# Optimization experiments

Measured on AMD Instinct MI355X. Metric: run time of the kernel, lower is better.

Reference implementation:

```python
import jax, jax.numpy as jnp
import numpy as np

N_HEADS = 8
N_LAYERS = 2
LN_EPS = 1e-5


def _mha(x, Win, bin_, Wout, bout):
    # torch nn.MultiheadAttention, eval mode (dropout off). x: [b, s, d]
    b, s, d = x.shape
    dh = d // N_HEADS
    qkv = x @ Win.T + bin_                      # [b, s, 3d]
    q, k, v = jnp.split(qkv, 3, axis=-1)
    q = q.reshape(b, s, N_HEADS, dh)
    k = k.reshape(b, s, N_HEADS, dh)
    v = v.reshape(b, s, N_HEADS, dh)
    scores = jnp.einsum('bqhd,bkhd->bhqk', q, k) / jnp.sqrt(jnp.asarray(dh, x.dtype))
    attn = jax.nn.softmax(scores, axis=-1)
    o = jnp.einsum('bhqk,bkhd->bqhd', attn, v).reshape(b, s, d)
    return o @ Wout.T + bout


def _layer_norm(x, g, b):
    mu = jnp.mean(x, axis=-1, keepdims=True)
    var = jnp.mean(jnp.square(x - mu), axis=-1, keepdims=True)
    return (x - mu) * jax.lax.rsqrt(var + LN_EPS) * g + b


def _vertex_conv(feat, inc, prev, Win, bin_, Wout, bout, Wproj, ln_g, ln_b, alpha):
    # feat: [b,m,d], inc: [b,m,e]
    attn = _mha(feat, Win, bin_, Wout, bout)              # [b,m,d]
    scores = jnp.einsum('bme,bmd->bed', inc, attn)        # incidence aggregation
    w = jax.nn.softmax(scores, axis=1)                    # softmax over edges
    # fused form of einsum('bme,bmd->bmed') then einsum('bmed,bed->bed')
    edge = scores * w                                     # [b,e,d]
    edge = edge @ Wproj.T                                 # no-bias projection
    edge = _layer_norm(edge, ln_g, ln_b)
    if prev is not None:
        edge = alpha * prev + (1.0 - alpha) * edge
        edge = edge + prev
    return edge


def _edge_conv(inc, edge_feat, prev, Win, bin_, Wout, bout, Wproj, ln_g, ln_b, alpha):
    # inc: [b,m,e], edge_feat: [b,e,d]
    _ = _mha(edge_feat, Win, bin_, Wout, bout)            # attn computed, output unused downstream
    wef = jnp.einsum('bed,bme->bmd', edge_feat, inc)      # edge->node aggregation
    node = wef @ Wproj.T
    node = _layer_norm(node, ln_g, ln_b)
    if prev is not None:
        node = alpha * prev + (1.0 - alpha) * node
        node = node + prev
    return node


def setup_inputs() -> dict:
    key = jax.random.key(0)
    ks = jax.random.split(key, 8)
    b, m, e, d = 8, 1024, 1536, 256
    s = 0.02
    return {
        'features': jax.random.normal(ks[0], (b, m, d), jnp.float32),
        'inc_mat': (jax.random.uniform(ks[1], (b, m, e), jnp.float32) < 0.05).astype(jnp.float32),
        'vc_Win': jax.random.normal(ks[2], (3 * d, d), jnp.float32) * s,
        'vc_bin': jnp.zeros((3 * d,), jnp.float32),
        'vc_Wout': jax.random.normal(ks[3], (d, d), jnp.float32) * s,
        'vc_bout': jnp.zeros((d,), jnp.float32),
        'vc_Wproj': jax.random.normal(ks[4], (d, d), jnp.float32) * s,
        'vc_ln_g': jnp.ones((d,), jnp.float32),
        'vc_ln_b': jnp.zeros((d,), jnp.float32),
        'vc_alpha': jnp.asarray(0.5, jnp.float32),
        'ec_Win': jax.random.normal(ks[5], (3 * d, d), jnp.float32) * s,
        'ec_bin': jnp.zeros((3 * d,), jnp.float32),
        'ec_Wout': jax.random.normal(ks[6], (d, d), jnp.float32) * s,
        'ec_bout': jnp.zeros((d,), jnp.float32),
        'ec_Wproj': jax.random.normal(ks[7], (d, d), jnp.float32) * s,
        'ec_ln_g': jnp.ones((d,), jnp.float32),
        'ec_ln_b': jnp.zeros((d,), jnp.float32),
        'ec_alpha': jnp.asarray(0.5, jnp.float32),
    }


def reference(features, inc_mat,
              vc_Win, vc_bin, vc_Wout, vc_bout, vc_Wproj, vc_ln_g, vc_ln_b, vc_alpha,
              ec_Win, ec_bin, ec_Wout, ec_bout, ec_Wproj, ec_ln_g, ec_ln_b, ec_alpha):
    vc = (vc_Win, vc_bin, vc_Wout, vc_bout, vc_Wproj, vc_ln_g, vc_ln_b, vc_alpha)
    ec = (ec_Win, ec_bin, ec_Wout, ec_bout, ec_Wproj, ec_ln_g, ec_ln_b, ec_alpha)
    edge_feats = _vertex_conv(features, inc_mat, None, *vc)
    node_feats = _edge_conv(inc_mat, edge_feats, features, *ec)
    for _ in range(N_LAYERS):  # shared weights across layers, as in the torch module
        edge_feats = _vertex_conv(features, inc_mat, edge_feats, *vc)
        node_feats = _edge_conv(inc_mat, edge_feats, node_feats, *ec)
    return node_feats, edge_feats, inc_mat
```

## Files before the change

kernel.cpp:

```cpp
#include <hip/hip_runtime.h>
#include <stdint.h>


#define DEV static __device__ __forceinline__

typedef __attribute__((ext_vector_type(8))) short bf16x8;
typedef __attribute__((ext_vector_type(4))) float f32x4;

DEV uint16_t f2bf(float x){
  union{float f; uint32_t u;} v; v.f=x;
  uint32_t r = v.u + 0x7fffu + ((v.u>>16)&1u);
  return (uint16_t)(r>>16);
}
DEV float bf2f(uint16_t b){
  union{uint32_t u; float f;} v; v.u=((uint32_t)b)<<16; return v.f;
}

DEV uint32_t cvtpk_bf16(float lo, float hi){
  uint32_t d;
  asm("v_cvt_pk_bf16_f32 %0, %1, %2" : "=v"(d) : "v"(lo), "v"(hi));
  return d;
}

#if __has_builtin(__builtin_amdgcn_exp2f)
DEV float exp2fast(float x){ return __builtin_amdgcn_exp2f(x); }
#else
DEV float exp2fast(float x){ return __expf(x * 0.6931471805599453f); }
#endif

#if __has_builtin(__builtin_amdgcn_global_load_lds)
#define HAVE_GLL 1
#else
#define HAVE_GLL 0
#endif

DEV void load_lds16(const uint16_t* g, void* l){
#if HAVE_GLL
  __builtin_amdgcn_global_load_lds((const __attribute__((address_space(1))) uint32_t*)g,
                                   (__attribute__((address_space(3))) uint32_t*)l, 16, 0, 0);
#else
  *(bf16x8*)l = *(const bf16x8*)g;
#endif
}

__global__ __launch_bounds__(256)
void prep(const float* __restrict__ inc, float* __restrict__ out_inc,
          uint16_t* __restrict__ incb, uint16_t* __restrict__ incT,
          const float* __restrict__ feats, const float* __restrict__ win,
          const float* __restrict__ wout, const float* __restrict__ wpv,
          const float* __restrict__ wpe,
          uint16_t* __restrict__ xb, uint16_t* __restrict__ ow,
          uint16_t* __restrict__ oo, uint16_t* __restrict__ ov,
          uint16_t* __restrict__ oe){
  __shared__ float T[32][33];
  int bx = blockIdx.x;
  int tid = threadIdx.x;
  if (bx < 12288){
    int x = bx % 48;
    int t = bx / 48;
    int y = t % 32;
    int b = t / 32;
    int c0 = x*32, r0 = y*32;
    int tx = tid & 31, ty = tid >> 5;
    size_t base = (size_t)b*1024*1536;
#pragma unroll
    for (int j=0;j<4;++j){
      int r = r0 + ty + j*8;
      size_t idx = base + (size_t)r*1536 + c0 + tx;
      float v = inc[idx];
      T[ty+j*8][tx] = v;
      out_inc[idx] = v;
      incb[idx] = f2bf(v);
    }
    __syncthreads();
    size_t baseT = (size_t)b*1536*1024;
#pragma unroll
    for (int j=0;j<4;++j){
      int c = c0 + ty + j*8;
      incT[baseT + (size_t)c*1024 + r0 + tx] = f2bf(T[tx][ty+j*8]);
    }
  } else {
    int i = (bx - 12288)*256 + tid;
    const float* src; uint16_t* dst; int j;
    if (i < 524288){ src=feats; dst=xb; j=i; }
    else {
      i -= 524288;
      if (i < 49152){ src=win; dst=ow; j=i; }
      else if (i < 65536){ src=wout; dst=oo; j=i-49152; }
      else if (i < 81920){ src=wpv; dst=ov; j=i-65536; }
      else { src=wpe; dst=oe; j=i-81920; }
    }
    float4 v = ((const float4*)src)[j];
    union { uint16_t u[4]; uint64_t q; } p;
    p.u[0]=f2bf(v.x); p.u[1]=f2bf(v.y); p.u[2]=f2bf(v.z); p.u[3]=f2bf(v.w);
    ((uint64_t*)dst)[j] = p.q;
  }
}

template<int WM, int BK, int EPI>
__global__ __launch_bounds__(256, 3)
void gemm_nt(const uint16_t* __restrict__ A, const uint16_t* __restrict__ B,
             float* __restrict__ Cf, uint16_t* __restrict__ Cb,
             const float* __restrict__ bias,
             int M, int N, int K, long sA, long sB, long sC,
             float* __restrict__ extra){
  constexpr int AROWS = WM*32;
  constexpr int UPR = BK/8;
  constexpr int RPP = 256/UPR;
  __shared__ short As[AROWS*BK];
  __shared__ short Bs[128*BK];
  const int tid = threadIdx.x;
  const int lane = tid & 63;
  const int w = tid >> 6;
  const int wm = w & 1, wn = w >> 1;
  const int r = lane & 15, q = lane >> 4;
  const long zb = blockIdx.z;
  const uint16_t* Ab = A + zb*sA + (size_t)(blockIdx.x*AROWS)*K;
  const uint16_t* Bb = B + zb*sB + (size_t)(blockIdx.y*128)*K;
  f32x4 acc[WM][4];
#pragma unroll
  for (int i=0;i<WM;++i)
#pragma unroll
    for (int j=0;j<4;++j) acc[i][j] = (f32x4){0.f,0.f,0.f,0.f};

  const int srow = tid / UPR;
  const int sblk = tid % UPR;

  for (int kb = 0; kb < K; kb += BK){
#pragma unroll
    for (int i=0;i<AROWS/RPP;++i){
      int row = srow + RPP*i;
      int lblk = sblk ^ (row & (UPR-1));
      load_lds16(Ab + (size_t)row*K + kb + lblk*8, (char*)As + i*4096 + tid*16);
    }
#pragma unroll
    for (int i=0;i<128/RPP;++i){
      int row = srow + RPP*i;
      int lblk = sblk ^ (row & (UPR-1));
      load_lds16(Bb + (size_t)row*K + kb + lblk*8, (char*)Bs + i*4096 + tid*16);
    }
    __syncthreads();
#pragma unroll
    for (int kc=0;kc<BK/32;++kc){
      bf16x8 af[WM], bf[4];
#pragma unroll
      for (int mt=0;mt<WM;++mt){
        int m = wm*(WM*16) + mt*16 + r;
        af[mt] = *(const bf16x8*)&As[m*BK + ((kc*4 + q) ^ (m&(UPR-1)))*8];
      }
#pragma unroll
      for (int nt=0;nt<4;++nt){
        int n = wn*64 + nt*16 + r;
        bf[nt] = *(const bf16x8*)&Bs[n*BK + ((kc*4 + q) ^ (n&(UPR-1)))*8];
      }
#pragma unroll
      for (int mt=0;mt<WM;++mt)
#pragma unroll
        for (int nt=0;nt<4;++nt)
          acc[mt][nt] = __builtin_amdgcn_mfma_f32_16x16x32_bf16(af[mt], bf[nt], acc[mt][nt], 0,0,0);
    }
    __syncthreads();
  }

  const int gm0 = blockIdx.x*AROWS + wm*(WM*16);
  const int gn0 = blockIdx.y*128 + wn*64;

  if constexpr (EPI == 1){
#pragma unroll
    for (int mt=0;mt<WM;++mt){
      int gmb = gm0 + mt*16 + q*4;
      size_t bb_ = (size_t)(gmb>>10)*(256*1024);
      int mm = gmb & 1023;
#pragma unroll
      for (int nt=0;nt<4;++nt){
        int gn = gn0 + nt*16 + r;
        float bv = bias ? bias[gn] : 0.f;
        union{uint16_t u[4]; uint64_t q64;} pk;
#pragma unroll
        for (int reg=0;reg<4;++reg) pk.u[reg] = f2bf(acc[mt][nt][reg] + bv);
        *(uint64_t*)(Cb + bb_ + (size_t)gn*1024 + mm) = pk.q64;
      }
    }
  } else {
#pragma unroll
    for (int mt=0;mt<WM;++mt){
#pragma unroll
      for (int nt=0;nt<4;++nt){
        int gn = gn0 + nt*16 + r;
        float bv = bias ? bias[gn] : 0.f;
#pragma unroll
        for (int reg=0;reg<4;++reg){
          int gm = gm0 + mt*16 + q*4 + reg;
          float v = acc[mt][nt][reg] + bv;
          size_t off = (size_t)(zb*sC) + (size_t)gm*N + gn;
          if (Cf) Cf[off] = v;
          if (Cb) Cb[off] = f2bf(v);
        }
      }
    }
  }
  (void)extra;
}

__global__ __launch_bounds__(256, 4)
void gemm_score(const uint16_t* __restrict__ A,
                const uint16_t* __restrict__ B,
                float* __restrict__ part,
                uint16_t* __restrict__ VE){
  __shared__ short As[32*64];
  __shared__ short Bs[256*64];
  const int tid = threadIdx.x;
  const int lane = tid & 63;
  const int w = tid >> 6;
  const int r = lane & 15, q = lane >> 4;
  const int bx = (blockIdx.x & 7)*48 + (blockIdx.x >> 3);
  const int batch = bx / 48;
  const uint16_t* Ab = A + (size_t)bx*32*1024;
  const uint16_t* Bb = B + (size_t)batch*256*1024;

  f32x4 acc[2][4];
#pragma unroll
  for (int i=0;i<2;++i)
#pragma unroll
    for (int j=0;j<4;++j) acc[i][j] = (f32x4){0.f,0.f,0.f,0.f};

  const int srow = tid >> 3;
  const int sblk = tid & 7;

  for (int kb = 0; kb < 1024; kb += 64){
    { int lblk = sblk ^ (srow & 7);
      load_lds16(Ab + (size_t)srow*1024 + kb + lblk*8, (char*)As + tid*16); }
#pragma unroll
    for (int i=0;i<8;++i){
      int row = srow + 32*i;
      int lblk = sblk ^ (row & 7);
      load_lds16(Bb + (size_t)row*1024 + kb + lblk*8, (char*)Bs + i*4096 + tid*16);
    }
    __syncthreads();
#pragma unroll
    for (int kc=0;kc<2;++kc){
      bf16x8 af[2], bf[4];
#pragma unroll
      for (int mt=0;mt<2;++mt){
        int m = mt*16 + r;
        af[mt] = *(const bf16x8*)&As[m*64 + ((kc*4 + q) ^ (m&7))*8];
      }
#pragma unroll
      for (int nt=0;nt<4;++nt){
        int n = w*64 + nt*16 + r;
        bf[nt] = *(const bf16x8*)&Bs[n*64 + ((kc*4 + q) ^ (n&7))*8];
      }
#pragma unroll
      for (int mt=0;mt<2;++mt)
#pragma unroll
        for (int nt=0;nt<4;++nt)
          acc[mt][nt] = __builtin_amdgcn_mfma_f32_16x16x32_bf16(af[mt], bf[nt], acc[mt][nt], 0,0,0);
    }
    __syncthreads();
  }

#pragma unroll
  for (int nt=0;nt<4;++nt){
    int gn = w*64 + nt*16 + r;
    float s = 0.f;
#pragma unroll
    for (int mt=0;mt<2;++mt){
#pragma unroll
      for (int reg=0;reg<4;++reg){
        float v = acc[mt][nt][reg];
        float ev = __expf(v);
        s += ev;
        int row = mt*16 + q*4 + reg;
        VE[(size_t)(bx*32 + row)*256 + gn] = f2bf(v*ev);
      }
    }
    s += __shfl_xor(s, 16);
    s += __shfl_xor(s, 32);
    if (q == 0) part[(size_t)bx*256 + gn] = s;
  }
}

__global__ __launch_bounds__(256, 4)
void gemm_ln_edge(const uint16_t* __restrict__ SB, const uint16_t* __restrict__ B,
                  const float* __restrict__ part, const float* __restrict__ g,
                  const float* __restrict__ bb, const float* __restrict__ alpha,
                  float* __restrict__ out, uint16_t* __restrict__ baset){
  __shared__ short As[32*64];
  __shared__ short Bs[256*64];
  __shared__ float lnS[4][32], lnQ[4][32];
  __shared__ float PLinv[256];
  const int tid = threadIdx.x;
  const int lane = tid & 63;
  const int w = tid >> 6;
  const int r = lane & 15, q = lane >> 4;
  const int bx = (blockIdx.x & 7)*48 + (blockIdx.x >> 3);
  const int batch = bx / 48;

  {
    float s = 0.f;
#pragma unroll
    for (int i=0;i<48;++i) s += part[((size_t)batch*48 + i)*256 + tid];
    PLinv[tid] = 1.0f / s;
  }
  __syncthreads();

  f32x4 acc[2][4];
#pragma unroll
  for (int i=0;i<2;++i)
#pragma unroll
    for (int j=0;j<4;++j) acc[i][j] = (f32x4){0.f,0.f,0.f,0.f};

  const int srow = tid >> 3;
  const int sblk = tid & 7;

  for (int kb = 0; kb < 256; kb += 64){
    {
      bf16x8 v = *(const bf16x8*)(SB + (size_t)(bx*32 + srow)*256 + kb + sblk*8);
      const float* Lp = &PLinv[kb + sblk*8];
      float xv[8];
#pragma unroll
      for (int j=0;j<8;++j) xv[j] = bf2f((uint16_t)v[j]) * Lp[j];
      union{uint32_t u[4]; bf16x8 v8;} pk;
      pk.u[0] = cvtpk_bf16(xv[0], xv[1]);
      pk.u[1] = cvtpk_bf16(xv[2], xv[3]);
      pk.u[2] = cvtpk_bf16(xv[4], xv[5]);
      pk.u[3] = cvtpk_bf16(xv[6], xv[7]);
      *(bf16x8*)&As[srow*64 + (sblk ^ (srow&7))*8] = pk.v8;
    }
#pragma unroll
    for (int i=0;i<8;++i){
      int row = srow + 32*i;
      int lblk = sblk ^ (row & 7);
      load_lds16(B + (size_t)row*256 + kb + lblk*8, (char*)Bs + i*4096 + tid*16);
    }
    __syncthreads();
#pragma unroll
    for (int kc=0;kc<2;++kc){
      bf16x8 af[2], bf[4];
#pragma unroll
      for (int mt=0;mt<2;++mt){
        int m = mt*16 + r;
        af[mt] = *(const bf16x8*)&As[m*64 + ((kc*4 + q) ^ (m&7))*8];
      }
#pragma unroll
      for (int nt=0;nt<4;++nt){
        int n = w*64 + nt*16 + r;
        bf[nt] = *(const bf16x8*)&Bs[n*64 + ((kc*4 + q) ^ (n&7))*8];
      }
#pragma unroll
      for (int mt=0;mt<2;++mt)
#pragma unroll
        for (int nt=0;nt<4;++nt)
          acc[mt][nt] = __builtin_amdgcn_mfma_f32_16x16x32_bf16(af[mt], bf[nt], acc[mt][nt], 0,0,0);
    }
    __syncthreads();
  }

  float rs[2][4], rq[2][4];
#pragma unroll
  for (int mt=0;mt<2;++mt)
#pragma unroll
    for (int reg=0;reg<4;++reg){
      float s=0.f, s2=0.f;
#pragma unroll
      for (int nt=0;nt<4;++nt){
        float v = acc[mt][nt][reg];
        s += v; s2 += v*v;
      }
#pragma unroll
      for (int off=1; off<16; off<<=1){ s += __shfl_xor(s,off); s2 += __shfl_xor(s2,off); }
      rs[mt][reg]=s; rq[mt][reg]=s2;
    }
  if (r == 0){
#pragma unroll
    for (int mt=0;mt<2;++mt)
#pragma unroll
      for (int reg=0;reg<4;++reg){
        int row = mt*16 + q*4 + reg;
        lnS[w][row] = rs[mt][reg];
        lnQ[w][row] = rq[mt][reg];
      }
  }
  __syncthreads();

  const float c0 = 3.0f + alpha[0];
  float mu_[2][4], rstd_[2][4];
#pragma unroll
  for (int mt=0;mt<2;++mt)
#pragma unroll
    for (int reg=0;reg<4;++reg){
      int row = mt*16 + q*4 + reg;
      float S = lnS[0][row]+lnS[1][row]+lnS[2][row]+lnS[3][row];
      float Q = lnQ[0][row]+lnQ[1][row]+lnQ[2][row]+lnQ[3][row];
      float mu = S * (1.f/256.f);
      float var = fmaxf(Q*(1.f/256.f) - mu*mu, 0.f);
      mu_[mt][reg] = mu;
      rstd_[mt][reg] = rsqrtf(var + 1e-5f);
    }

  int e0 = (bx % 48) * 32;
#pragma unroll
  for (int mt=0;mt<2;++mt){
#pragma unroll
    for (int nt=0;nt<4;++nt){
      int gn = w*64 + nt*16 + r;
      float gv = g[gn], bv = bb[gn];
      union{uint16_t u[4]; uint64_t q64;} pk;
#pragma unroll
      for (int reg=0;reg<4;++reg){
        int row = mt*16 + q*4 + reg;
        size_t gm = (size_t)bx*32 + row;
        float o = ((acc[mt][nt][reg]-mu_[mt][reg])*rstd_[mt][reg]*gv + bv) * c0;
        pk.u[reg] = f2bf(o);
        out[gm*256 + gn] = o;
      }
      int ee = e0 + mt*16 + q*4;
      *(uint64_t*)(baset + ((size_t)batch*256 + gn)*1536 + ee) = pk.q64;
    }
  }
}

__global__ __launch_bounds__(256, 3)
void gemm_node_fused(const uint16_t* __restrict__ inc,
                     const uint16_t* __restrict__ baset,
                     const uint16_t* __restrict__ wpe,
                     const float* __restrict__ g, const float* __restrict__ bb,
                     const float* __restrict__ alpha,
                     const float* __restrict__ feats, float* __restrict__ out){
  __shared__ short Ws[256*64];
  __shared__ short As2[32*256];
  __shared__ short Is[32*64];
  const int tid = threadIdx.x;
  const int lane = tid & 63;
  const int w = tid >> 6;
  const int r = lane & 15, q = lane >> 4;
  const int bx = (blockIdx.x & 7)*32 + (blockIdx.x >> 3);
  const int batch = bx >> 5;
  const int mt0 = (bx & 31) * 32;

  const int srow = tid >> 3;
  const int sblk = tid & 7;

  const uint16_t* Bb = baset + (size_t)batch*256*1536;
  const uint16_t* Ib = inc + ((size_t)batch*1024 + mt0)*1536;

  f32x4 acc1[4][2];
#pragma unroll
  for (int i=0;i<4;++i)
#pragma unroll
    for (int j=0;j<2;++j) acc1[i][j] = (f32x4){0.f,0.f,0.f,0.f};

  for (int kb = 0; kb < 1536; kb += 64){
#pragma unroll
    for (int i=0;i<8;++i){
      int row = srow + 32*i;
      int lblk = sblk ^ (row & 7);
      load_lds16(Bb + (size_t)row*1536 + kb + lblk*8, (char*)Ws + i*4096 + tid*16);
    }
    { int lblk = sblk ^ (srow & 7);
      load_lds16(Ib + (size_t)srow*1536 + kb + lblk*8, (char*)Is + tid*16); }
    __syncthreads();
#pragma unroll
    for (int kc=0;kc<2;++kc){
      bf16x8 af[4], bf[2];
#pragma unroll
      for (int mt=0;mt<4;++mt){
        int d = w*64 + mt*16 + r;
        af[mt] = *(const bf16x8*)&Ws[d*64 + ((kc*4 + q) ^ (d&7))*8];
      }
#pragma unroll
      for (int nt=0;nt<2;++nt){
        int m = nt*16 + r;
        bf[nt] = *(const bf16x8*)&Is[m*64 + ((kc*4 + q) ^ (m&7))*8];
      }
#pragma unroll
      for (int mt=0;mt<4;++mt)
#pragma unroll
        for (int nt=0;nt<2;++nt)
          acc1[mt][nt] = __builtin_amdgcn_mfma_f32_16x16x32_bf16(af[mt], bf[nt], acc1[mt][nt], 0,0,0);
    }
    __syncthreads();
  }

#pragma unroll
  for (int mt=0;mt<4;++mt){
    int j = w*8 + mt*2 + (q>>1);
#pragma unroll
    for (int nt=0;nt<2;++nt){
      int m = nt*16 + r;
      union{uint16_t u[4]; uint64_t q64;} pk;
#pragma unroll
      for (int reg=0;reg<4;++reg) pk.u[reg] = f2bf(acc1[mt][nt][reg]);
      *(uint64_t*)((char*)As2 + m*512 + ((j ^ (m&7))<<4) + ((q&1)<<3)) = pk.q64;
    }
  }

  f32x4 acc2[4][2];
#pragma unroll
  for (int i=0;i<4;++i)
#pragma unroll
    for (int j=0;j<2;++j) acc2[i][j] = (f32x4){0.f,0.f,0.f,0.f};

  for (int kb = 0; kb < 256; kb += 64){
#pragma unroll
    for (int i=0;i<8;++i){
      int row = srow + 32*i;
      int lblk = sblk ^ (row & 7);
      load_lds16(wpe + (size_t)row*256 + kb + lblk*8, (char*)Ws + i*4096 + tid*16);
    }
    __syncthreads();
#pragma unroll
    for (int kc=0;kc<2;++kc){
      bf16x8 af[4], bf[2];
#pragma unroll
      for (int mt=0;mt<4;++mt){
        int dp = w*64 + mt*16 + r;
        af[mt] = *(const bf16x8*)&Ws[dp*64 + ((kc*4 + q) ^ (dp&7))*8];
      }
#pragma unroll
      for (int nt=0;nt<2;++nt){
        int m = nt*16 + r;
        int jr = (kb>>3) + kc*4 + q;
        bf[nt] = *(const bf16x8*)((char*)As2 + m*512 + ((jr ^ (m&7))<<4));
      }
#pragma unroll
      for (int mt=0;mt<4;++mt)
#pragma unroll
        for (int nt=0;nt<2;++nt)
          acc2[mt][nt] = __builtin_amdgcn_mfma_f32_16x16x32_bf16(af[mt], bf[nt], acc2[mt][nt], 0,0,0);
    }
    __syncthreads();
  }

  float* lnS = (float*)Is;
  float* lnQ = lnS + 128;
  float s_[2], q_[2];
#pragma unroll
  for (int nt=0;nt<2;++nt){
    float s=0.f, s2=0.f;
#pragma unroll
    for (int mt=0;mt<4;++mt)
#pragma unroll
      for (int reg=0;reg<4;++reg){
        float v = acc2[mt][nt][reg];
        s += v; s2 += v*v;
      }
    s += __shfl_xor(s,16); s2 += __shfl_xor(s2,16);
    s += __shfl_xor(s,32); s2 += __shfl_xor(s2,32);
    s_[nt]=s; q_[nt]=s2;
  }
  if (q == 0){
#pragma unroll
    for (int nt=0;nt<2;++nt){
      lnS[w*32 + nt*16 + r] = s_[nt];
      lnQ[w*32 + nt*16 + r] = q_[nt];
    }
  }
  __syncthreads();

  const float a = alpha[0];
  const float ap1 = 1.f + a;
  const float cn = (1.f - a)*(ap1*ap1 + ap1 + 1.f);
  const float cf = ap1*ap1*ap1;

  float mu_[2], rstd_[2];
#pragma unroll
  for (int nt=0;nt<2;++nt){
    int col = nt*16 + r;
    float S = lnS[col] + lnS[32+col] + lnS[64+col] + lnS[96+col];
    float Q = lnQ[col] + lnQ[32+col] + lnQ[64+col] + lnQ[96+col];
    float mu = S * (1.f/256.f);
    float var = fmaxf(Q*(1.f/256.f) - mu*mu, 0.f);
    mu_[nt] = mu;
    rstd_[nt] = rsqrtf(var + 1e-5f);
  }

#pragma unroll
  for (int mt=0;mt<4;++mt){
    int dp0 = w*64 + mt*16 + q*4;
    float4 gv = *(const float4*)&g[dp0];
    float4 bv = *(const float4*)&bb[dp0];
#pragma unroll
    for (int nt=0;nt<2;++nt){
      int m = nt*16 + r;
      size_t gm = (size_t)batch*1024 + mt0 + m;
      float4 fv = *(const float4*)&feats[gm*256 + dp0];
      float4 ov;
      ov.x = cf*fv.x + cn*((acc2[mt][nt][0]-mu_[nt])*rstd_[nt]*gv.x + bv.x);
      ov.y = cf*fv.y + cn*((acc2[mt][nt][1]-mu_[nt])*rstd_[nt]*gv.y + bv.y);
      ov.z = cf*fv.z + cn*((acc2[mt][nt][2]-mu_[nt])*rstd_[nt]*gv.z + bv.z);
      ov.w = cf*fv.w + cn*((acc2[mt][nt][3]-mu_[nt])*rstd_[nt]*gv.w + bv.w);
      *(float4*)&out[gm*256 + dp0] = ov;
    }
  }
}

DEV void stage_K(short* Kl, const uint16_t* __restrict__ qkv, size_t rowbase,
                 int c, int h, int kr){
  const uint16_t* kp = qkv + ((rowbase + c*256 + kr)*768 + 256 + h*32);
  int sz = (kr&3) ^ ((kr>>2)&1);
#pragma unroll
  for (int lb=0; lb<4; ++lb){
    bf16x8 v = *(const bf16x8*)(kp + lb*8);
    *(bf16x8*)&Kl[kr*32 + ((lb ^ sz))*8] = v;
  }
}

DEV void stage_V(short* VT, const uint16_t* __restrict__ qkv, size_t rowbase,
                 int c, int h, int t){
  int kvp = (t>>1)*2;
  int dhh = (t&1)*16;
  const uint16_t* v0 = qkv + ((rowbase + c*256 + kvp)*768 + 512 + h*32 + dhh);
  const uint16_t* v1 = v0 + 768;
  bf16x8 a0 = *(const bf16x8*)(v0);
  bf16x8 a1 = *(const bf16x8*)(v0+8);
  bf16x8 b0 = *(const bf16x8*)(v1);
  bf16x8 b1 = *(const bf16x8*)(v1+8);
  int blkbase = kvp>>3, off = kvp&7;
#pragma unroll
  for (int i=0;i<8;++i){
    int dh = dhh + i;
    uint32_t pack = (uint32_t)(uint16_t)a0[i] | ((uint32_t)(uint16_t)b0[i]<<16);
    *(uint32_t*)&VT[dh*256 + ((blkbase ^ (dh&7))*8) + off] = pack;
  }
#pragma unroll
  for (int i=0;i<8;++i){
    int dh = dhh + 8 + i;
    uint32_t pack = (uint32_t)(uint16_t)a1[i] | ((uint32_t)(uint16_t)b1[i]<<16);
    *(uint32_t*)&VT[dh*256 + ((blkbase ^ (dh&7))*8) + off] = pack;
  }
}

__global__ __launch_bounds__(512)
void attn_fwd(const uint16_t* __restrict__ qkv, uint16_t* __restrict__ O){
  __shared__ short Kl[256*32];
  __shared__ short VT[32*256];
  __shared__ short Pl[8][16*36];
  const int tid = threadIdx.x, lane = tid&63, w = tid>>6;
  const int r = lane&15, q = lane>>4;
  const int logical = (blockIdx.x & 7)*64 + (blockIdx.x >> 3);
  const int bh = logical >> 3, qc = logical & 7;
  const int b = bh>>3, h = bh&7;
  const int q0 = qc*128 + w*16;
  const size_t rowbase = (size_t)b*1024;

  bf16x8 aq;
  {
    const float qscale = 0.25505654380651023f;
    const uint16_t* p = qkv + ((rowbase + q0 + r)*768 + h*32 + q*8);
    bf16x8 t = *(const bf16x8*)p;
#pragma unroll
    for (int j=0;j<8;++j)
      t[j] = (short)f2bf(bf2f((uint16_t)t[j]) * qscale);
    aq = t;
  }

  f32x4 o[2];
  o[0]=(f32x4){0.f,0.f,0.f,0.f}; o[1]=(f32x4){0.f,0.f,0.f,0.f};
  float l = 0.f;

  for (int c=0;c<4;++c){
    __syncthreads();
    if (tid < 256) stage_K(Kl, qkv, rowbase, c, h, tid);
    else           stage_V(VT, qkv, rowbase, c, h, tid-256);
    __syncthreads();
    for (int s32=0; s32<8; ++s32){
#pragma unroll
      for (int t2=0;t2<2;++t2){
        int rn = s32*32 + t2*16 + r;
        int sz = (rn&3) ^ ((rn>>2)&1);
        bf16x8 bk = *(const bf16x8*)&Kl[rn*32 + ((q ^ sz))*8];
        f32x4 z = (f32x4){0.f,0.f,0.f,0.f};
        f32x4 st = __builtin_amdgcn_mfma_f32_16x16x32_bf16(bk, aq, z, 0,0,0);
        float p0 = exp2fast(st[0]);
        float p1 = exp2fast(st[1]);
        float p2 = exp2fast(st[2]);
        float p3 = exp2fast(st[3]);
        l += (p0+p1)+(p2+p3);
        union{uint32_t u[2]; uint64_t q64;} pk;
        pk.u[0] = cvtpk_bf16(p0, p1);
        pk.u[1] = cvtpk_bf16(p2, p3);
        *(uint64_t*)&Pl[w][r*36 + t2*16 + q*4] = pk.q64;
      }
      bf16x8 bv[2];
#pragma unroll
      for (int db=0;db<2;++db){
        int dh = db*16 + r;
        bv[db] = *(const bf16x8*)&VT[dh*256 + (((s32*4 + q) ^ (dh&7)))*8];
      }
      bf16x8 ap = *(const bf16x8*)&Pl[w][r*36 + q*8];
#pragma unroll
      for (int db=0;db<2;++db)
        o[db] = __builtin_amdgcn_mfma_f32_16x16x32_bf16(ap, bv[db], o[db], 0,0,0);
    }
  }

  l += __shfl_xor(l, 16);
  l += __shfl_xor(l, 32);
#pragma unroll
  for (int db=0;db<2;++db)
#pragma unroll
    for (int reg=0;reg<4;++reg){
      float li = __shfl(l, q*4 + reg);
      int qr = q0 + q*4 + reg;
      O[(rowbase + qr)*256 + h*32 + db*16 + r] = f2bf(o[db][reg] / li);
    }
}

extern "C" void kernel_launch(void* const* d_in, const int* in_sizes, int n_in,
                              void* d_out, int out_size, void* d_ws, size_t ws_size,
                              hipStream_t stream){
  const float* features = (const float*)d_in[0];
  const float* inc      = (const float*)d_in[1];
  const float* vc_Win   = (const float*)d_in[2];
  const float* vc_bin   = (const float*)d_in[3];
  const float* vc_Wout  = (const float*)d_in[4];
  const float* vc_bout  = (const float*)d_in[5];
  const float* vc_Wproj = (const float*)d_in[6];
  const float* vc_ln_g  = (const float*)d_in[7];
  const float* vc_ln_b  = (const float*)d_in[8];
  const float* vc_alpha = (const float*)d_in[9];
  const float* ec_Wproj = (const float*)d_in[14];
  const float* ec_ln_g  = (const float*)d_in[15];
  const float* ec_ln_b  = (const float*)d_in[16];
  const float* ec_alpha = (const float*)d_in[17];

  float* out = (float*)d_out;
  float* out_node = out;
  float* out_edge = out + 2097152;
  float* out_inc  = out + 5242880;

  char* ws = (char*)d_ws;
  uint16_t* XB     = (uint16_t*)(ws + 0);
  float*    PART   = (float*)   (ws + 0);
  uint16_t* WINB   = (uint16_t*)(ws + 4194304);
  uint16_t* WOUTB  = (uint16_t*)(ws + 4587520);
  uint16_t* WPVB   = (uint16_t*)(ws + 4718592);
  uint16_t* WPEB   = (uint16_t*)(ws + 4849664);
  uint16_t* INCB   = (uint16_t*)(ws + 4988928);
  uint16_t* INCT   = (uint16_t*)(ws + 30154752);
  uint16_t* QKVB   = (uint16_t*)(ws + 55320576);
  uint16_t* SCORESB= (uint16_t*)(ws + 55320576);
  uint16_t* OB     = (uint16_t*)(ws + 67903488);
  uint16_t* ATTNT  = (uint16_t*)(ws + 72097792);
  uint16_t* BASET  = (uint16_t*)(ws + 82583552);

  prep<<<14720,256,0,stream>>>(inc, out_inc, INCB, INCT,
                               features, vc_Win, vc_Wout, vc_Wproj, ec_Wproj,
                               XB, WINB, WOUTB, WPVB, WPEB);

  gemm_nt<4,64,0><<<dim3(64,6,1),256,0,stream>>>(XB, WINB, nullptr, QKVB, vc_bin,
                                                 8192,768,256, 0,0,0, nullptr);
  attn_fwd<<<512,512,0,stream>>>(QKVB, OB);
  gemm_nt<2,128,1><<<dim3(128,2,1),256,0,stream>>>(OB, WOUTB, nullptr, ATTNT, vc_bout,
                                                   8192,256,256, 0,0,0, nullptr);

  gemm_score<<<384,256,0,stream>>>(INCT, ATTNT, PART, SCORESB);

  gemm_ln_edge<<<384,256,0,stream>>>(SCORESB, WPVB, PART, vc_ln_g, vc_ln_b,
                                     vc_alpha, out_edge, BASET);

  gemm_node_fused<<<256,256,0,stream>>>(INCB, BASET, WPEB, ec_ln_g, ec_ln_b,
                                        ec_alpha, features, out_node);
}
```

Measured before the change: 256.7 us.

## Load GEMM fragments directly from global memory instead of staging through LDS

Replaces the LDS-staged tiling in the QKV/output projections, score GEMM, edge LN GEMM and fused node GEMM with direct per-lane 16-byte global loads of MFMA fragments, dropping the shared buffers and most barriers. The QKV GEMM is retiled to 64-row blocks with more blocks. It also adds s_setprio around MFMAs in the attention kernel. This removes LDS traffic and synchronisation, and may raise occupancy through lower LDS use. The cost is losing tile reuse across waves, so global/L2 traffic goes up and loads become strided per lane.

```diff
diff --git a/kernel.cpp b/kernel.cpp
--- a/kernel.cpp
+++ b/kernel.cpp
@@ -27,21 +27,6 @@
 #else
 DEV float exp2fast(float x){ return __expf(x * 0.6931471805599453f); }
 #endif
-
-#if __has_builtin(__builtin_amdgcn_global_load_lds)
-#define HAVE_GLL 1
-#else
-#define HAVE_GLL 0
-#endif
-
-DEV void load_lds16(const uint16_t* g, void* l){
-#if HAVE_GLL
-  __builtin_amdgcn_global_load_lds((const __attribute__((address_space(1))) uint32_t*)g,
-                                   (__attribute__((address_space(3))) uint32_t*)l, 16, 0, 0);
-#else
-  *(bf16x8*)l = *(const bf16x8*)g;
-#endif
-}
 
 __global__ __launch_bounds__(256)
 void prep(const float* __restrict__ inc, float* __restrict__ out_inc,
@@ -97,77 +82,52 @@
   }
 }
 
-template<int WM, int BK, int EPI>
-__global__ __launch_bounds__(256, 3)
-void gemm_nt(const uint16_t* __restrict__ A, const uint16_t* __restrict__ B,
-             float* __restrict__ Cf, uint16_t* __restrict__ Cb,
-             const float* __restrict__ bias,
-             int M, int N, int K, long sA, long sB, long sC,
-             float* __restrict__ extra){
-  constexpr int AROWS = WM*32;
-  constexpr int UPR = BK/8;
-  constexpr int RPP = 256/UPR;
-  __shared__ short As[AROWS*BK];
-  __shared__ short Bs[128*BK];
+template<int EPI>
+__global__ __launch_bounds__(256, 4)
+void gemm_nt_d(const uint16_t* __restrict__ A, const uint16_t* __restrict__ B,
+               uint16_t* __restrict__ Cb, const float* __restrict__ bias,
+               int N, int K){
   const int tid = threadIdx.x;
   const int lane = tid & 63;
   const int w = tid >> 6;
   const int wm = w & 1, wn = w >> 1;
   const int r = lane & 15, q = lane >> 4;
-  const long zb = blockIdx.z;
-  const uint16_t* Ab = A + zb*sA + (size_t)(blockIdx.x*AROWS)*K;
-  const uint16_t* Bb = B + zb*sB + (size_t)(blockIdx.y*128)*K;
-  f32x4 acc[WM][4];
-#pragma unroll
-  for (int i=0;i<WM;++i)
+
+  const uint16_t* apm[2];
+  const uint16_t* bpn[4];
+#pragma unroll
+  for (int mt=0;mt<2;++mt)
+    apm[mt] = A + (size_t)(blockIdx.x*64 + wm*32 + mt*16 + r)*K + q*8;
+#pragma unroll
+  for (int nt=0;nt<4;++nt)
+    bpn[nt] = B + (size_t)(blockIdx.y*128 + wn*64 + nt*16 + r)*K + q*8;
+
+  f32x4 acc[2][4];
+#pragma unroll
+  for (int i=0;i<2;++i)
 #pragma unroll
     for (int j=0;j<4;++j) acc[i][j] = (f32x4){0.f,0.f,0.f,0.f};
 
-  const int srow = tid / UPR;
-  const int sblk = tid % UPR;
-
-  for (int kb = 0; kb < K; kb += BK){
-#pragma unroll
-    for (int i=0;i<AROWS/RPP;++i){
-      int row = srow + RPP*i;
-      int lblk = sblk ^ (row & (UPR-1));
-      load_lds16(Ab + (size_t)row*K + kb + lblk*8, (char*)As + i*4096 + tid*16);
-    }
-#pragma unroll
-    for (int i=0;i<128/RPP;++i){
-      int row = srow + RPP*i;
-      int lblk = sblk ^ (row & (UPR-1));
-      load_lds16(Bb + (size_t)row*K + kb + lblk*8, (char*)Bs + i*4096 + tid*16);
-    }
-    __syncthreads();
-#pragma unroll
-    for (int kc=0;kc<BK/32;++kc){
-      bf16x8 af[WM], bf[4];
-#pragma unroll
-      for (int mt=0;mt<WM;++mt){
-        int m = wm*(WM*16) + mt*16 + r;
-        af[mt] = *(const bf16x8*)&As[m*BK + ((kc*4 + q) ^ (m&(UPR-1)))*8];
-      }
-#pragma unroll
-      for (int nt=0;nt<4;++nt){
-        int n = wn*64 + nt*16 + r;
-        bf[nt] = *(const bf16x8*)&Bs[n*BK + ((kc*4 + q) ^ (n&(UPR-1)))*8];
-      }
-#pragma unroll
-      for (int mt=0;mt<WM;++mt)
-#pragma unroll
-        for (int nt=0;nt<4;++nt)
-          acc[mt][nt] = __builtin_amdgcn_mfma_f32_16x16x32_bf16(af[mt], bf[nt], acc[mt][nt], 0,0,0);
-    }
-    __syncthreads();
-  }
-
-  const int gm0 = blockIdx.x*AROWS + wm*(WM*16);
+#pragma unroll 4
+  for (int kb=0; kb<K; kb+=32){
+    bf16x8 af[2], bf[4];
+#pragma unroll
+    for (int mt=0;mt<2;++mt) af[mt] = *(const bf16x8*)(apm[mt] + kb);
+#pragma unroll
+    for (int nt=0;nt<4;++nt) bf[nt] = *(const bf16x8*)(bpn[nt] + kb);
+#pragma unroll
+    for (int mt=0;mt<2;++mt)
+#pragma unroll
+      for (int nt=0;nt<4;++nt)
+        acc[mt][nt] = __builtin_amdgcn_mfma_f32_16x16x32_bf16(af[mt], bf[nt], acc[mt][nt], 0,0,0);
+  }
+
+  const int gm0 = blockIdx.x*64 + wm*32;
   const int gn0 = blockIdx.y*128 + wn*64;
 
   if constexpr (EPI == 1){
 #pragma unroll
-    for (int mt=0;mt<WM;++mt){
+    for (int mt=0;mt<2;++mt){
       int gmb = gm0 + mt*16 + q*4;
       size_t bb_ = (size_t)(gmb>>10)*(256*1024);
       int mm = gmb & 1023;
@@ -183,7 +143,7 @@
     }
   } else {
 #pragma unroll
-    for (int mt=0;mt<WM;++mt){
+    for (int mt=0;mt<2;++mt){
 #pragma unroll
       for (int nt=0;nt<4;++nt){
         int gn = gn0 + nt*16 + r;
@@ -191,15 +151,11 @@
 #pragma unroll
         for (int reg=0;reg<4;++reg){
           int gm = gm0 + mt*16 + q*4 + reg;
-          float v = acc[mt][nt][reg] + bv;
-          size_t off = (size_t)(zb*sC) + (size_t)gm*N + gn;
-          if (Cf) Cf[off] = v;
-          if (Cb) Cb[off] = f2bf(v);
+          Cb[(size_t)gm*N + gn] = f2bf(acc[mt][nt][reg] + bv);
         }
       }
     }
   }
-  (void)extra;
 }
 
 __global__ __launch_bounds__(256, 4)
@@ -207,16 +163,21 @@
                 const uint16_t* __restrict__ B,
                 float* __restrict__ part,
                 uint16_t* __restrict__ VE){
-  __shared__ short As[32*64];
-  __shared__ short Bs[256*64];
   const int tid = threadIdx.x;
   const int lane = tid & 63;
   const int w = tid >> 6;
   const int r = lane & 15, q = lane >> 4;
   const int bx = (blockIdx.x & 7)*48 + (blockIdx.x >> 3);
   const int batch = bx / 48;
-  const uint16_t* Ab = A + (size_t)bx*32*1024;
-  const uint16_t* Bb = B + (size_t)batch*256*1024;
+
+  const uint16_t* apm[2];
+  const uint16_t* bpn[4];
+#pragma unroll
+  for (int mt=0;mt<2;++mt)
+    apm[mt] = A + (size_t)(bx*32 + mt*16 + r)*1024 + q*8;
+#pragma unroll
+  for (int nt=0;nt<4;++nt)
+    bpn[nt] = B + (size_t)(batch*256 + w*64 + nt*16 + r)*1024 + q*8;
 
   f32x4 acc[2][4];
 #pragma unroll
@@ -224,39 +185,18 @@
 #pragma unroll
     for (int j=0;j<4;++j) acc[i][j] = (f32x4){0.f,0.f,0.f,0.f};
 
-  const int srow = tid >> 3;
-  const int sblk = tid & 7;
-
-  for (int kb = 0; kb < 1024; kb += 64){
-    { int lblk = sblk ^ (srow & 7);
-      load_lds16(Ab + (size_t)srow*1024 + kb + lblk*8, (char*)As + tid*16); }
-#pragma unroll
-    for (int i=0;i<8;++i){
-      int row = srow + 32*i;
-      int lblk = sblk ^ (row & 7);
-      load_lds16(Bb + (size_t)row*1024 + kb + lblk*8, (char*)Bs + i*4096 + tid*16);
-    }
-    __syncthreads();
-#pragma unroll
-    for (int kc=0;kc<2;++kc){
-      bf16x8 af[2], bf[4];
-#pragma unroll
-      for (int mt=0;mt<2;++mt){
-        int m = mt*16 + r;
-        af[mt] = *(const bf16x8*)&As[m*64 + ((kc*4 + q) ^ (m&7))*8];
-      }
-#pragma unroll
-      for (int nt=0;nt<4;++nt){
-        int n = w*64 + nt*16 + r;
-        bf[nt] = *(const bf16x8*)&Bs[n*64 + ((kc*4 + q) ^ (n&7))*8];
-      }
-#pragma unroll
-      for (int mt=0;mt<2;++mt)
-#pragma unroll
-        for (int nt=0;nt<4;++nt)
-          acc[mt][nt] = __builtin_amdgcn_mfma_f32_16x16x32_bf16(af[mt], bf[nt], acc[mt][nt], 0,0,0);
-    }
-    __syncthreads();
+#pragma unroll 4
+  for (int kb=0; kb<1024; kb+=32){
+    bf16x8 af[2], bf[4];
+#pragma unroll
+    for (int mt=0;mt<2;++mt) af[mt] = *(const bf16x8*)(apm[mt] + kb);
+#pragma unroll
+    for (int nt=0;nt<4;++nt) bf[nt] = *(const bf16x8*)(bpn[nt] + kb);
+#pragma unroll
+    for (int mt=0;mt<2;++mt)
+#pragma unroll
+      for (int nt=0;nt<4;++nt)
+        acc[mt][nt] = __builtin_amdgcn_mfma_f32_16x16x32_bf16(af[mt], bf[nt], acc[mt][nt], 0,0,0);
   }
 
 #pragma unroll
@@ -286,7 +226,6 @@
                   const float* __restrict__ bb, const float* __restrict__ alpha,
                   float* __restrict__ out, uint16_t* __restrict__ baset){
   __shared__ short As[32*64];
-  __shared__ short Bs[256*64];
   __shared__ float lnS[4][32], lnQ[4][32];
   __shared__ float PLinv[256];
   const int tid = threadIdx.x;
@@ -313,6 +252,11 @@
   const int srow = tid >> 3;
   const int sblk = tid & 7;
 
+  const uint16_t* bpn[4];
+#pragma unroll
+  for (int nt=0;nt<4;++nt)
+    bpn[nt] = B + (size_t)(w*64 + nt*16 + r)*256 + q*8;
+
   for (int kb = 0; kb < 256; kb += 64){
     {
       bf16x8 v = *(const bf16x8*)(SB + (size_t)(bx*32 + srow)*256 + kb + sblk*8);
@@ -327,12 +271,6 @@
       pk.u[3] = cvtpk_bf16(xv[6], xv[7]);
       *(bf16x8*)&As[srow*64 + (sblk ^ (srow&7))*8] = pk.v8;
     }
-#pragma unroll
-    for (int i=0;i<8;++i){
-      int row = srow + 32*i;
-      int lblk = sblk ^ (row & 7);
-      load_lds16(B + (size_t)row*256 + kb + lblk*8, (char*)Bs + i*4096 + tid*16);
-    }
     __syncthreads();
 #pragma unroll
     for (int kc=0;kc<2;++kc){
@@ -343,10 +281,8 @@
         af[mt] = *(const bf16x8*)&As[m*64 + ((kc*4 + q) ^ (m&7))*8];
       }
 #pragma unroll
-      for (int nt=0;nt<4;++nt){
-        int n = w*64 + nt*16 + r;
-        bf[nt] = *(const bf16x8*)&Bs[n*64 + ((kc*4 + q) ^ (n&7))*8];
-      }
+      for (int nt=0;nt<4;++nt)
+        bf[nt] = *(const bf16x8*)(bpn[nt] + kb + kc*32);
 #pragma unroll
       for (int mt=0;mt<2;++mt)
 #pragma unroll
@@ -427,9 +363,8 @@
                      const float* __restrict__ g, const float* __restrict__ bb,
                      const float* __restrict__ alpha,
                      const float* __restrict__ feats, float* __restrict__ out){
-  __shared__ short Ws[256*64];
   __shared__ short As2[32*256];
-  __shared__ short Is[32*64];
+  __shared__ float lnSQ[256];
   const int tid = threadIdx.x;
   const int lane = tid & 63;
   const int w = tid >> 6;
@@ -438,11 +373,14 @@
   const int batch = bx >> 5;
   const int mt0 = (bx & 31) * 32;
 
-  const int srow = tid >> 3;
-  const int sblk = tid & 7;
-
-  const uint16_t* Bb = baset + (size_t)batch*256*1536;
-  const uint16_t* Ib = inc + ((size_t)batch*1024 + mt0)*1536;
+  const uint16_t* apm[4];
+  const uint16_t* bpn[2];
+#pragma unroll
+  for (int mt=0;mt<4;++mt)
+    apm[mt] = baset + (size_t)(batch*256 + w*64 + mt*16 + r)*1536 + q*8;
+#pragma unroll
+  for (int nt=0;nt<2;++nt)
+    bpn[nt] = inc + (size_t)(batch*1024 + mt0 + nt*16 + r)*1536 + q*8;
 
   f32x4 acc1[4][2];
 #pragma unroll
@@ -450,36 +388,18 @@
 #pragma unroll
     for (int j=0;j<2;++j) acc1[i][j] = (f32x4){0.f,0.f,0.f,0.f};
 
-  for (int kb = 0; kb < 1536; kb += 64){
-#pragma unroll
-    for (int i=0;i<8;++i){
-      int row = srow + 32*i;
-      int lblk = sblk ^ (row & 7);
-      load_lds16(Bb + (size_t)row*1536 + kb + lblk*8, (char*)Ws + i*4096 + tid*16);
-    }
-    { int lblk = sblk ^ (srow & 7);
-      load_lds16(Ib + (size_t)srow*1536 + kb + lblk*8, (char*)Is + tid*16); }
-    __syncthreads();
-#pragma unroll
-    for (int kc=0;kc<2;++kc){
-      bf16x8 af[4], bf[2];
-#pragma unroll
-      for (int mt=0;mt<4;++mt){
-        int d = w*64 + mt*16 + r;
-        af[mt] = *(const bf16x8*)&Ws[d*64 + ((kc*4 + q) ^ (d&7))*8];
-      }
-#pragma unroll
-      for (int nt=0;nt<2;++nt){
-        int m = nt*16 + r;
-        bf[nt] = *(const bf16x8*)&Is[m*64 + ((kc*4 + q) ^ (m&7))*8];
-      }
-#pragma unroll
-      for (int mt=0;mt<4;++mt)
-#pragma unroll
-        for (int nt=0;nt<2;++nt)
-          acc1[mt][nt] = __builtin_amdgcn_mfma_f32_16x16x32_bf16(af[mt], bf[nt], acc1[mt][nt], 0,0,0);
-    }
-    __syncthreads();
+#pragma unroll 4
+  for (int kb = 0; kb < 1536; kb += 32){
+    bf16x8 af[4], bf[2];
+#pragma unroll
+    for (int mt=0;mt<4;++mt) af[mt] = *(const bf16x8*)(apm[mt] + kb);
+#pragma unroll
+    for (int nt=0;nt<2;++nt) bf[nt] = *(const bf16x8*)(bpn[nt] + kb);
+#pragma unroll
+    for (int mt=0;mt<4;++mt)
+#pragma unroll
+      for (int nt=0;nt<2;++nt)
+        acc1[mt][nt] = __builtin_amdgcn_mfma_f32_16x16x32_bf16(af[mt], bf[nt], acc1[mt][nt], 0,0,0);
   }
 
 #pragma unroll
@@ -494,6 +414,7 @@
       *(uint64_t*)((char*)As2 + m*512 + ((j ^ (m&7))<<4) + ((q&1)<<3)) = pk.q64;
     }
   }
+  __syncthreads();
 
   f32x4 acc2[4][2];
 #pragma unroll
@@ -501,39 +422,31 @@
 #pragma unroll
     for (int j=0;j<2;++j) acc2[i][j] = (f32x4){0.f,0.f,0.f,0.f};
 
-  for (int kb = 0; kb < 256; kb += 64){
-#pragma unroll
-    for (int i=0;i<8;++i){
-      int row = srow + 32*i;
-      int lblk = sblk ^ (row & 7);
-      load_lds16(wpe + (size_t)row*256 + kb + lblk*8, (char*)Ws + i*4096 + tid*16);
-    }
-    __syncthreads();
-#pragma unroll
-    for (int kc=0;kc<2;++kc){
-      bf16x8 af[4], bf[2];
-#pragma unroll
-      for (int mt=0;mt<4;++mt){
-        int dp = w*64 + mt*16 + r;
-        af[mt] = *(const bf16x8*)&Ws[dp*64 + ((kc*4 + q) ^ (dp&7))*8];
-      }
-#pragma unroll
-      for (int nt=0;nt<2;++nt){
-        int m = nt*16 + r;
-        int jr = (kb>>3) + kc*4 + q;
-        bf[nt] = *(const bf16x8*)((char*)As2 + m*512 + ((jr ^ (m&7))<<4));
-      }
-#pragma unroll
-      for (int mt=0;mt<4;++mt)
-#pragma unroll
-        for (int nt=0;nt<2;++nt)
-          acc2[mt][nt] = __builtin_amdgcn_mfma_f32_16x16x32_bf16(af[mt], bf[nt], acc2[mt][nt], 0,0,0);
-    }
-    __syncthreads();
-  }
-
-  float* lnS = (float*)Is;
-  float* lnQ = lnS + 128;
+  const uint16_t* wpm[4];
+#pragma unroll
+  for (int mt=0;mt<4;++mt)
+    wpm[mt] = wpe + (size_t)(w*64 + mt*16 + r)*256 + q*8;
+
+#pragma unroll
+  for (int kb = 0; kb < 256; kb += 32){
+    bf16x8 af[4], bf[2];
+#pragma unroll
+    for (int mt=0;mt<4;++mt) af[mt] = *(const bf16x8*)(wpm[mt] + kb);
+#pragma unroll
+    for (int nt=0;nt<2;++nt){
+      int m = nt*16 + r;
+      int jr = (kb>>3) + q;
+      bf[nt] = *(const bf16x8*)((char*)As2 + m*512 + ((jr ^ (m&7))<<4));
+    }
+#pragma unroll
+    for (int mt=0;mt<4;++mt)
+#pragma unroll
+      for (int nt=0;nt<2;++nt)
+        acc2[mt][nt] = __builtin_amdgcn_mfma_f32_16x16x32_bf16(af[mt], bf[nt], acc2[mt][nt], 0,0,0);
+  }
+
+  float* lnS = lnSQ;
+  float* lnQ = lnSQ + 128;
   float s_[2], q_[2];
 #pragma unroll
   for (int nt=0;nt<2;++nt){
@@ -549,6 +462,7 @@
     s += __shfl_xor(s,32); s2 += __shfl_xor(s2,32);
     s_[nt]=s; q_[nt]=s2;
   }
+  __syncthreads();
   if (q == 0){
 #pragma unroll
     for (int nt=0;nt<2;++nt){
@@ -671,7 +585,9 @@
         int sz = (rn&3) ^ ((rn>>2)&1);
         bf16x8 bk = *(const bf16x8*)&Kl[rn*32 + ((q ^ sz))*8];
         f32x4 z = (f32x4){0.f,0.f,0.f,0.f};
+        __builtin_amdgcn_s_setprio(1);
         f32x4 st = __builtin_amdgcn_mfma_f32_16x16x32_bf16(bk, aq, z, 0,0,0);
+        __builtin_amdgcn_s_setprio(0);
         float p0 = exp2fast(st[0]);
         float p1 = exp2fast(st[1]);
         float p2 = exp2fast(st[2]);
@@ -689,9 +605,11 @@
         bv[db] = *(const bf16x8*)&VT[dh*256 + (((s32*4 + q) ^ (dh&7)))*8];
       }
       bf16x8 ap = *(const bf16x8*)&Pl[w][r*36 + q*8];
+      __builtin_amdgcn_s_setprio(1);
 #pragma unroll
       for (int db=0;db<2;++db)
         o[db] = __builtin_amdgcn_mfma_f32_16x16x32_bf16(ap, bv[db], o[db], 0,0,0);
+      __builtin_amdgcn_s_setprio(0);
     }
   }
 
@@ -749,11 +667,9 @@
                                features, vc_Win, vc_Wout, vc_Wproj, ec_Wproj,
                                XB, WINB, WOUTB, WPVB, WPEB);
 
-  gemm_nt<4,64,0><<<dim3(64,6,1),256,0,stream>>>(XB, WINB, nullptr, QKVB, vc_bin,
-                                                 8192,768,256, 0,0,0, nullptr);
+  gemm_nt_d<0><<<dim3(128,6,1),256,0,stream>>>(XB, WINB, QKVB, vc_bin, 768, 256);
   attn_fwd<<<512,512,0,stream>>>(QKVB, OB);
-  gemm_nt<2,128,1><<<dim3(128,2,1),256,0,stream>>>(OB, WOUTB, nullptr, ATTNT, vc_bout,
-                                                   8192,256,256, 0,0,0, nullptr);
+  gemm_nt_d<1><<<dim3(128,2,1),256,0,stream>>>(OB, WOUTB, ATTNT, vc_bout, 256, 256);
 
   gemm_score<<<384,256,0,stream>>>(INCT, ATTNT, PART, SCORESB);
 
```

After: 328.2 us. 27.9% more time.
